# Performance work log

Hardware: AMD Instinct MI355X
Metric: run time of the kernel (lower is better)

The kernel has to match this reference:

```python
import jax, jax.numpy as jnp
import numpy as np

B, S, N, C = 8, 256, 256, 64
NH = 8
H, W = 256, 256
D = N * C // NH  # per-head channel dim = 2048
EPS = 1e-12


def window_reverse(windows, ws, Hh, Ww, Cc):
    # windows: (B, S, N, C) -> (B, H*W, C)
    b = windows.shape[0]
    x = windows.reshape(b, Hh // ws[0], Ww // ws[1], ws[0], ws[1], Cc)
    x = x.transpose(0, 1, 3, 2, 4, 5).reshape(b, Hh, Ww, Cc).reshape(b, Hh * Ww, Cc)
    return x


def window_partition(x, ws):
    # x: (B, H, W, C) -> (B, nWin, winElems, C)
    b, hh, ww, cc = x.shape
    x = x.reshape(b, hh // ws[0], ws[0], ww // ws[1], ws[1], cc)
    return x.transpose(0, 1, 3, 2, 4, 5).reshape(b, (hh // ws[0]) * (ww // ws[1]), ws[0] * ws[1], cc)


def setup_inputs() -> dict:
    key = jax.random.key(0)
    ks = jax.random.split(key, 6)
    x = jax.random.normal(ks[0], (B, S, N, C), dtype=jnp.float32)
    qkv_w = jax.random.normal(ks[1], (4 * C, C), dtype=jnp.float32) * 0.02
    qkv_b = jnp.zeros((4 * C,), dtype=jnp.float32)
    proj_w = jax.random.normal(ks[2], (C, C), dtype=jnp.float32) * 0.02
    proj_b = jnp.zeros((C,), dtype=jnp.float32)
    temperature1 = jnp.ones((NH, 1, 1), dtype=jnp.float32)
    temperature2 = jnp.ones((NH, 1, 1), dtype=jnp.float32)
    return {"x": x, "qkv_w": qkv_w, "qkv_b": qkv_b, "proj_w": proj_w,
            "proj_b": proj_b, "temperature1": temperature1, "temperature2": temperature2}


def reference(x, qkv_w, qkv_b, proj_w, proj_b, temperature1, temperature2):
    b, s, n, c = x.shape
    xf = x.reshape(b, s * n, c)
    # fused 4-way qkv projection (q, k, v_H, v_V)
    qkvv = (xf @ qkv_w.T + qkv_b).reshape(b, s, 4, NH, D).transpose(2, 0, 3, 1, 4)
    q, k, v_H, v_V = qkvv[0], qkvv[1], qkvv[2], qkvv[3]  # each (B, NH, S, D)

    # reorient v_V from H-windows (columns) to V-windows (rows)
    v_V = v_V.transpose(0, 2, 1, 3).reshape(b, s, n, c)       # (B,S,N,C)
    v_V = v_V.transpose(0, 2, 1, 3)                           # (B,N,S,C)
    v_V = window_reverse(v_V, (H, 1), H, W, c).reshape(b, H, W, c)
    v_V = window_partition(v_V, (1, W))                       # (B,H,W,C)
    v_V = v_V.transpose(0, 2, 1, 3)                           # (B,W,H,C) == (B,S,N,C)
    v_V = v_V.reshape(b, s, NH, D).transpose(0, 2, 1, 3)      # (B,NH,S,D)

    # cosine attention over S with per-head temperature
    qn = q / jnp.maximum(jnp.linalg.norm(q, axis=-1, keepdims=True), EPS)
    kn = k / jnp.maximum(jnp.linalg.norm(k, axis=-1, keepdims=True), EPS)
    sim = jnp.einsum('bhsd,bhtd->bhst', qn, kn)  # (B,NH,S,S)
    attn_H = jax.nn.softmax(sim * temperature1, axis=-1)
    attn_V = jax.nn.softmax(sim * temperature2, axis=-1)

    x_H = jnp.einsum('bhst,bhtd->bhsd', attn_H, v_H).transpose(0, 2, 1, 3).reshape(b, s * n, c)
    x_V = jnp.einsum('bhst,bhtd->bhsd', attn_V, v_V).transpose(0, 2, 1, 3).reshape(b, s * n, c)

    out = (x_H + x_V) @ proj_w.T + proj_b
    return out.reshape(b, s, n, c)
```

## Files before the change

kernel.cpp:

```cpp
#include <hip/hip_runtime.h>


using half_t = _Float16;
using half4 = __attribute__((ext_vector_type(4))) _Float16;
using half8 = __attribute__((ext_vector_type(8))) _Float16;
using f32x4 = __attribute__((ext_vector_type(4))) float;

#define NTOK 524288

#define GLDS(g, l) __builtin_amdgcn_global_load_lds( \
    (const __attribute__((address_space(1))) void*)(g), \
    (__attribute__((address_space(3))) void*)(l), 16, 0, 0)

#define WS_Q      0
#define WS_K      67108864
#define WS_VH     134217728
#define WS_VV     201326592
#define WS_XHV    268435456
#define WS_NQ     335544320
#define WS_NK     335609856
#define WS_WH     335675392
#define WS_WP     335708160

__global__ void kW0(const float* __restrict__ qkv_w, const float* __restrict__ proj_w,
                    half_t* __restrict__ Wh, half_t* __restrict__ Wp) {
    int tid = threadIdx.x;
    for (int i = tid; i < 256 * 64; i += 256) Wh[i] = (half_t)qkv_w[i];
    for (int i = tid; i < 64 * 64; i += 256) Wp[i] = (half_t)proj_w[i];
}

__device__ inline void y_tile_mfma(const float* __restrict__ xb,
                                   const half_t* __restrict__ Wh,
                                   int tbase, int hi, int lo,
                                   f32x4 (&acc)[4][4], int wave, int lane) {
    const int l15 = lane & 15, quad = lane >> 4;
#pragma unroll
    for (int kc = 0; kc < 2; ++kc) {
        const int c = kc * 32 + quad * 8;
        half8 afr[4];
#pragma unroll
        for (int mt = 0; mt < 4; ++mt) {
            int m = mt * 16 + l15;
            int token = tbase + (m >> 3) * hi + (m & 7) * lo;
            const float* p = xb + (size_t)token * 64 + c;
            f32x4 f0 = *(const f32x4*)p;
            f32x4 f1 = *(const f32x4*)(p + 4);
            half8 a;
            a[0] = (half_t)f0[0]; a[1] = (half_t)f0[1]; a[2] = (half_t)f0[2]; a[3] = (half_t)f0[3];
            a[4] = (half_t)f1[0]; a[5] = (half_t)f1[1]; a[6] = (half_t)f1[2]; a[7] = (half_t)f1[3];
            afr[mt] = a;
        }
#pragma unroll
        for (int i = 0; i < 4; ++i) {
            int j = (wave * 4 + i) * 16 + l15;
            half8 bfr = *(const half8*)(Wh + j * 64 + c);
#pragma unroll
            for (int mt = 0; mt < 4; ++mt)
                acc[mt][i] = __builtin_amdgcn_mfma_f32_16x16x32_f16(afr[mt], bfr, acc[mt][i], 0, 0, 0);
        }
    }
}

__device__ inline void y_tile_mfma_swapped(const float* __restrict__ xb,
                                           const half_t* __restrict__ Wh,
                                           int tbase, int hi, int lo,
                                           f32x4 (&acc)[4][4], int wave, int lane) {
    const int l15 = lane & 15, quad = lane >> 4;
#pragma unroll
    for (int kc = 0; kc < 2; ++kc) {
        const int c = kc * 32 + quad * 8;
        half8 bx[4];
#pragma unroll
        for (int mt = 0; mt < 4; ++mt) {
            int m = mt * 16 + l15;
            int token = tbase + (m >> 3) * hi + (m & 7) * lo;
            const float* p = xb + (size_t)token * 64 + c;
            f32x4 f0 = *(const f32x4*)p;
            f32x4 f1 = *(const f32x4*)(p + 4);
            half8 a;
            a[0] = (half_t)f0[0]; a[1] = (half_t)f0[1]; a[2] = (half_t)f0[2]; a[3] = (half_t)f0[3];
            a[4] = (half_t)f1[0]; a[5] = (half_t)f1[1]; a[6] = (half_t)f1[2]; a[7] = (half_t)f1[3];
            bx[mt] = a;
        }
#pragma unroll
        for (int i = 0; i < 4; ++i) {
            int j = (wave * 4 + i) * 16 + l15;
            half8 aw = *(const half8*)(Wh + j * 64 + c);
#pragma unroll
            for (int mt = 0; mt < 4; ++mt)
                acc[i][mt] = __builtin_amdgcn_mfma_f32_16x16x32_f16(aw, bx[mt], acc[i][mt], 0, 0, 0);
        }
    }
}

__device__ inline void y_dump_transposed(f32x4 (&acc)[4][4], const float* __restrict__ qkv_b,
                                         half_t* yldsT, int wave, int lane) {
    const int l15 = lane & 15, quad = lane >> 4;
#pragma unroll
    for (int i = 0; i < 4; ++i) {
        int j = (wave * 4 + i) * 16 + l15;
        float bj = qkv_b[j];
#pragma unroll
        for (int mt = 0; mt < 4; ++mt)
#pragma unroll
            for (int r = 0; r < 4; ++r)
                yldsT[j * 72 + mt * 16 + quad * 4 + r] = (half_t)(acc[mt][i][r] + bj);
    }
}

__global__ __launch_bounds__(256) void kA1(const float* __restrict__ x,
                                           const half_t* __restrict__ Wh,
                                           const float* __restrict__ qkv_b,
                                           half_t* __restrict__ Q, half_t* __restrict__ K,
                                           float* __restrict__ normQ, float* __restrict__ normK) {
    __shared__ half_t ylds[64 * 264];
    __shared__ float scr[256];
    int idx = blockIdx.x;
    int sb = idx & 31; idx >>= 5;
    int h = idx & 7; idx >>= 3;
    int g = idx & 1; int b = idx >> 1;
    int s0 = sb * 8;
    int n0 = g * 64 + h * 8;
    int tid = threadIdx.x, wave = tid >> 6, lane = tid & 63;
    const int l15 = lane & 15, quad = lane >> 4;
    const float* xb = x + (size_t)b * 65536 * 64;
    f32x4 acc[4][4];
#pragma unroll
    for (int a = 0; a < 4; ++a)
#pragma unroll
        for (int c = 0; c < 4; ++c) acc[a][c] = {0.f, 0.f, 0.f, 0.f};
    y_tile_mfma_swapped(xb, Wh, s0 * 256 + n0, 256, 1, acc, wave, lane);
#pragma unroll
    for (int i = 0; i < 4; ++i) {
        int j0 = (wave * 4 + i) * 16 + quad * 4;
        f32x4 bj = *(const f32x4*)&qkv_b[j0];
#pragma unroll
        for (int mt = 0; mt < 4; ++mt) {
            int m = mt * 16 + l15;
            half4 v;
#pragma unroll
            for (int r = 0; r < 4; ++r) v[r] = (half_t)(acc[i][mt][r] + bj[r]);
            *(half4*)&ylds[m * 264 + j0] = v;
        }
    }
    __syncthreads();
    half_t* dst = (g == 0 ? Q : K) + ((size_t)(b * 8 + h) * 256 + s0) * 2048;
    int ns = tid >> 5, jc = (tid & 31) * 8;
#pragma unroll
    for (int si = 0; si < 8; ++si) {
        half8 v = *(const half8*)&ylds[(si * 8 + ns) * 264 + jc];
        *(half8*)(dst + (size_t)si * 2048 + ns * 256 + jc) = v;
    }
    float sum = 0.f;
#pragma unroll
    for (int nn = 0; nn < 8; ++nn) {
        half8 v = *(const half8*)&ylds[((tid >> 5) * 8 + nn) * 264 + (tid & 31) * 8];
#pragma unroll
        for (int e = 0; e < 8; ++e) { float f = (float)v[e]; sum += f * f; }
    }
    scr[tid] = sum;
    __syncthreads();
    if (tid < 8) {
        float s = 0.f;
        for (int k2 = 0; k2 < 32; ++k2) s += scr[tid * 32 + k2];
        float* nd = (g == 0 ? normQ : normK);
        nd[(b * 8 + h) * 256 + s0 + tid] = s;
    }
}

__global__ __launch_bounds__(256) void kA2H(const float* __restrict__ x,
                                            const half_t* __restrict__ Wh,
                                            const float* __restrict__ qkv_b,
                                            half_t* __restrict__ VH) {
    __shared__ half_t yldsT[256 * 72];
    int idx = blockIdx.x;
    int sb = idx & 3; idx >>= 2;
    int nn = idx & 63; int b = idx >> 6;
    int h = nn >> 3, ns = nn & 7;
    int n = 128 + nn;
    int s0 = sb * 64;
    int tid = threadIdx.x, wave = tid >> 6, lane = tid & 63;
    const int l15 = lane & 15, quad = lane >> 4;
    const float* xb = x + (size_t)b * 65536 * 64;
    f32x4 acc[4][4];
#pragma unroll
    for (int a = 0; a < 4; ++a)
#pragma unroll
        for (int c = 0; c < 4; ++c) acc[a][c] = {0.f, 0.f, 0.f, 0.f};
    y_tile_mfma(xb, Wh, s0 * 256 + n, 2048, 256, acc, wave, lane);
#pragma unroll
    for (int i = 0; i < 4; ++i) {
        int j = (wave * 4 + i) * 16 + l15;
        float bj = qkv_b[j];
#pragma unroll
        for (int mt = 0; mt < 4; ++mt) {
            half4 v;
#pragma unroll
            for (int r = 0; r < 4; ++r) v[r] = (half_t)(acc[mt][i][r] + bj);
            *(half4*)&yldsT[j * 72 + mt * 16 + quad * 4] = v;
        }
    }
    __syncthreads();
    int jl = lane >> 3, tc = lane & 7;
    half_t* base = VH + ((size_t)(b * 8 + h) * 2048 + ns * 256) * 256 + s0 + tc * 8;
#pragma unroll
    for (int u = 0; u < 8; ++u) {
        int j = wave * 64 + u * 8 + jl;
        half8 v = *(const half8*)&yldsT[j * 72 + tc * 8];
        *(half8*)(base + (size_t)j * 256) = v;
    }
}

__global__ __launch_bounds__(256) void kA2V(const float* __restrict__ x,
                                            const half_t* __restrict__ Wh,
                                            const float* __restrict__ qkv_b,
                                            half_t* __restrict__ VV) {
    __shared__ half_t vlds[64 * 264];
    int idx = blockIdx.x;
    int st = idx & 255; int b = idx >> 8;
    int h = st >> 5;
    int tid = threadIdx.x, wave = tid >> 6, lane = tid & 63;
    const float* xb = x + (size_t)b * 65536 * 64;
    f32x4 acc[4][4];
#pragma unroll
    for (int a = 0; a < 4; ++a)
#pragma unroll
        for (int c = 0; c < 4; ++c) acc[a][c] = {0.f, 0.f, 0.f, 0.f};
    y_tile_mfma(xb, Wh, st * 256 + 192, 8, 1, acc, wave, lane);
    {
        const int l15 = lane & 15, quad = lane >> 4;
#pragma unroll
        for (int i = 0; i < 4; ++i) {
            int j = (wave * 4 + i) * 16 + l15;
            float bj = qkv_b[j];
            int dm = j & 63;
            int jc = j >> 6;
#pragma unroll
            for (int mt = 0; mt < 4; ++mt)
#pragma unroll
                for (int r = 0; r < 4; ++r) {
                    int m = mt * 16 + quad * 4 + r;
                    int t = 32 * (m >> 3) + 4 * (m & 7) + jc;
                    vlds[dm * 264 + t] = (half_t)(acc[mt][i][r] + bj);
                }
        }
    }
    __syncthreads();
    half_t* base = VV + ((size_t)(b * 8 + h) * 2048 + (st & 31) * 64) * 256;
    int l31 = lane & 31, lh = lane >> 5;
#pragma unroll
    for (int u = 0; u < 8; ++u) {
        int dm = u * 8 + wave * 2 + lh;
        half8 v = *(const half8*)&vlds[dm * 264 + l31 * 8];
        *(half8*)(base + (size_t)dm * 256 + l31 * 8) = v;
    }
}

__global__ __launch_bounds__(1024, 4) void kB(const half_t* __restrict__ Q, const half_t* __restrict__ K,
                                              const half_t* __restrict__ VH, const half_t* __restrict__ VV,
                                              const float* __restrict__ normQ, const float* __restrict__ normK,
                                              const float* __restrict__ temp1, const float* __restrict__ temp2,
                                              half_t* __restrict__ xhv) {
    extern __shared__ char smem[];
    half_t* PH = (half_t*)smem;
    half_t* PV = (half_t*)(smem + 40960);
    float* rq  = (float*)(smem + 122880);
    float* rk  = (float*)(smem + 123136);

    int idx = blockIdx.x;
    int bh = idx & 63;
    int sqb = idx >> 6;
    int h = bh & 7, b = bh >> 3;
    int sq0 = sqb * 64;
    int tid = threadIdx.x, wave = tid >> 6, lane = tid & 63;
    int l15 = lane & 15, quad = lane >> 4;
    float t1 = temp1[h], t2 = temp2[h];
    const half_t* Qb = Q + (size_t)bh * 256 * 2048;
    const half_t* Kb = K + (size_t)bh * 256 * 2048;
    const half_t* VHb = VH + (size_t)bh * 2048 * 256;
    const half_t* VVb = VV + (size_t)bh * 2048 * 256;

    if (tid < 64) rq[tid] = 1.f / fmaxf(sqrtf(normQ[bh * 256 + sq0 + tid]), 1e-12f);
    if (tid < 256) rk[tid] = 1.f / fmaxf(sqrtf(normK[bh * 256 + tid]), 1e-12f);

    {
        const int l7 = lane & 7, l8 = lane >> 3;
        const int swzh = (l7 ^ (l8 & 7)) * 8;
        const half_t* gK0 = Kb + (size_t)(wave * 8 + l8) * 2048 + swzh;
        const half_t* gK1 = Kb + (size_t)(128 + wave * 8 + l8) * 2048 + swzh;
        const half_t* gQ  = Qb + (size_t)(sq0 + (wave & 7) * 8 + l8) * 2048 + swzh;

        auto STAGE = [&](int kk, char* B) {
            const int off = kk * 64;
            GLDS(gK0 + off, B + wave * 1024);
            GLDS(gK1 + off, B + 16384 + wave * 1024);
            if (wave < 8) GLDS(gQ + off, B + 32768 + wave * 1024);
        };

        f32x4 acc1[4];
#pragma unroll
        for (int a = 0; a < 4; ++a) acc1[a] = {0.f, 0.f, 0.f, 0.f};
        const int tcol = wave * 16 + l15;
        const int ts7 = tcol & 7;

        auto COMPUTE = [&](const char* B) {
            const half_t* KsB = (const half_t*)B;
            const half_t* QsB = (const half_t*)(B + 32768);
#pragma unroll
            for (int sub = 0; sub < 2; ++sub) {
                int c16 = sub * 4 + quad;
                half8 bfr = *(const half8*)(KsB + tcol * 64 + (c16 ^ ts7) * 8);
#pragma unroll
                for (int mt = 0; mt < 4; ++mt) {
                    int m = mt * 16 + l15;
                    half8 afr = *(const half8*)(QsB + m * 64 + (c16 ^ (m & 7)) * 8);
                    acc1[mt] = __builtin_amdgcn_mfma_f32_16x16x32_f16(afr, bfr, acc1[mt], 0, 0, 0);
                }
            }
        };

        STAGE(0, smem);
        STAGE(1, smem + 40960);
        __syncthreads();
        int c0 = 0, c2 = 2;
        for (int kk = 0; kk < 30; ++kk) {
            COMPUTE(smem + c0 * 40960);
            STAGE(kk + 2, smem + c2 * 40960);
            if (wave < 8) { asm volatile("s_waitcnt vmcnt(3)" ::: "memory"); }
            else          { asm volatile("s_waitcnt vmcnt(2)" ::: "memory"); }
            __builtin_amdgcn_s_barrier();
            __builtin_amdgcn_sched_barrier(0);
            c0 = (c0 == 2) ? 0 : c0 + 1;
            c2 = (c2 == 2) ? 0 : c2 + 1;
        }
        COMPUTE(smem + c0 * 40960);
        asm volatile("s_waitcnt vmcnt(0)" ::: "memory");
        __builtin_amdgcn_s_barrier();
        __builtin_amdgcn_sched_barrier(0);
        c0 = (c0 == 2) ? 0 : c0 + 1;
        COMPUTE(smem + c0 * 40960);
        float rkt = rk[tcol];
#pragma unroll
        for (int mt = 0; mt < 4; ++mt)
#pragma unroll
            for (int r = 0; r < 4; ++r) {
                int row = mt * 16 + quad * 4 + r;
                PH[row * 264 + tcol] = (half_t)(acc1[mt][r] * rq[row] * rkt);
            }
    }
    __syncthreads();

    {
        int r_ = tid >> 4, cc = tid & 15;
        half_t* phrow = &PH[r_ * 264 + cc * 16];
        half_t* pvrow = &PV[r_ * 264 + cc * 16];
        half8 v0 = *(const half8*)phrow;
        half8 v1 = *(const half8*)(phrow + 8);
        float fv[16];
#pragma unroll
        for (int e = 0; e < 8; ++e) { fv[e] = (float)v0[e]; fv[8 + e] = (float)v1[e]; }
        float mx = fv[0], mn = fv[0];
#pragma unroll
        for (int e = 1; e < 16; ++e) { mx = fmaxf(mx, fv[e]); mn = fminf(mn, fv[e]); }
#pragma unroll
        for (int m = 1; m < 16; m <<= 1) {
            mx = fmaxf(mx, __shfl_xor(mx, m, 16));
            mn = fminf(mn, __shfl_xor(mn, m, 16));
        }
        float mh = (t1 >= 0.f) ? t1 * mx : t1 * mn;
        float mv = (t2 >= 0.f) ? t2 * mx : t2 * mn;
        float sh = 0.f, sv = 0.f;
#pragma unroll
        for (int e = 0; e < 16; ++e) {
            sh += __expf(fv[e] * t1 - mh);
            sv += __expf(fv[e] * t2 - mv);
        }
#pragma unroll
        for (int m = 1; m < 16; m <<= 1) {
            sh += __shfl_xor(sh, m, 16);
            sv += __shfl_xor(sv, m, 16);
        }
        float rh = 1.f / sh, rv = 1.f / sv;
        half8 o0, o1, p0, p1;
#pragma unroll
        for (int e = 0; e < 8; ++e) {
            o0[e] = (half_t)(__expf(fv[e] * t1 - mh) * rh);
            o1[e] = (half_t)(__expf(fv[8 + e] * t1 - mh) * rh);
            p0[e] = (half_t)(__expf(fv[e] * t2 - mv) * rv);
            p1[e] = (half_t)(__expf(fv[8 + e] * t2 - mv) * rv);
        }
        *(half8*)phrow = o0; *(half8*)(phrow + 8) = o1;
        *(half8*)pvrow = p0; *(half8*)(pvrow + 8) = p1;
    }
    __syncthreads();

    const int rr = lane >> 3, c8 = (lane & 7) * 8;
    half_t* myscr = (half_t*)(smem + 81920 + wave * 2560);
#pragma unroll
    for (int i2 = 0; i2 < 2; ++i2) {
        int d0 = wave * 64 + i2 * 1024;
        f32x4 acc2[4][4];
#pragma unroll
        for (int a = 0; a < 4; ++a)
#pragma unroll
            for (int c = 0; c < 4; ++c) acc2[a][c] = {0.f, 0.f, 0.f, 0.f};
        for (int kc = 0; kc < 8; ++kc) {
            int tk = kc * 32 + quad * 8;
            half8 afr[4];
#pragma unroll
            for (int mt = 0; mt < 4; ++mt)
                afr[mt] = *(const half8*)&PH[(mt * 16 + l15) * 264 + tk];
#pragma unroll
            for (int nt = 0; nt < 4; ++nt) {
                half8 bfr = *(const half8*)(VHb + (size_t)(d0 + nt * 16 + l15) * 256 + tk);
#pragma unroll
                for (int mt = 0; mt < 4; ++mt)
                    acc2[mt][nt] = __builtin_amdgcn_mfma_f32_16x16x32_f16(afr[mt], bfr, acc2[mt][nt], 0, 0, 0);
            }
#pragma unroll
            for (int mt = 0; mt < 4; ++mt)
                afr[mt] = *(const half8*)&PV[(mt * 16 + l15) * 264 + tk];
#pragma unroll
            for (int nt = 0; nt < 4; ++nt) {
                half8 bfr = *(const half8*)(VVb + (size_t)(d0 + nt * 16 + l15) * 256 + tk);
#pragma unroll
                for (int mt = 0; mt < 4; ++mt)
                    acc2[mt][nt] = __builtin_amdgcn_mfma_f32_16x16x32_f16(afr[mt], bfr, acc2[mt][nt], 0, 0, 0);
            }
        }
        int db = wave + i2 * 16;
        half_t* xbase = xhv + (((size_t)(b * 8 + h) * 32 + db) * 256 + sq0) * 64;
#pragma unroll
        for (int mt = 0; mt < 4; ++mt) {
#pragma unroll
            for (int nt = 0; nt < 4; ++nt)
#pragma unroll
                for (int r = 0; r < 4; ++r)
                    myscr[(quad * 4 + r) * 72 + nt * 16 + l15] = (half_t)acc2[mt][nt][r];
#pragma unroll
            for (int u = 0; u < 2; ++u) {
                half8 v = *(const half8*)&myscr[(u * 8 + rr) * 72 + c8];
                *(half8*)(xbase + (size_t)(mt * 16 + u * 8 + rr) * 64 + c8) = v;
            }
        }
    }
}

__global__ __launch_bounds__(256) void kC(const half_t* __restrict__ xhv, const half_t* __restrict__ Wp,
                                          const float* __restrict__ proj_b, float* __restrict__ out) {
    __shared__ float ot[64 * 68];
    int tid = threadIdx.x, wave = tid >> 6, lane = tid & 63;
    int l15 = lane & 15, quad = lane >> 4;
    size_t T0 = (size_t)blockIdx.x * 64;
    int b = (int)(T0 >> 16);
    int s = (int)((T0 >> 8) & 255);
    int n0 = (int)(T0 & 255);
    f32x4 acc[4];
#pragma unroll
    for (int a = 0; a < 4; ++a) acc[a] = {0.f, 0.f, 0.f, 0.f};
#pragma unroll
    for (int kc = 0; kc < 2; ++kc) {
        int c = kc * 32 + quad * 8;
        half8 bfr = *(const half8*)(Wp + (wave * 16 + l15) * 64 + c);
#pragma unroll
        for (int mt = 0; mt < 4; ++mt) {
            int n = n0 + mt * 16 + l15;
            int hh = n >> 5, db = n & 31;
            const half_t* arow = xhv + (((size_t)(b * 8 + hh) * 32 + db) * 256 + s) * 64;
            half8 afr = *(const half8*)(arow + c);
            acc[mt] = __builtin_amdgcn_mfma_f32_16x16x32_f16(afr, bfr, acc[mt], 0, 0, 0);
        }
    }
    float bj = proj_b[wave * 16 + l15];
#pragma unroll
    for (int mt = 0; mt < 4; ++mt)
#pragma unroll
        for (int r = 0; r < 4; ++r)
            ot[(mt * 16 + quad * 4 + r) * 68 + wave * 16 + l15] = acc[mt][r] + bj;
    __syncthreads();
    int row = tid >> 2;
#pragma unroll
    for (int u = 0; u < 4; ++u) {
        int col = (tid & 3) * 4 + u * 16;
        f32x4 v = *(const f32x4*)&ot[row * 68 + col];
        *(f32x4*)(out + (T0 + row) * 64 + col) = v;
    }
}

extern "C" void kernel_launch(void* const* d_in, const int* in_sizes, int n_in,
                              void* d_out, int out_size, void* d_ws, size_t ws_size,
                              hipStream_t stream) {
    const float* x      = (const float*)d_in[0];
    const float* qkv_w  = (const float*)d_in[1];
    const float* qkv_b  = (const float*)d_in[2];
    const float* proj_w = (const float*)d_in[3];
    const float* proj_b = (const float*)d_in[4];
    const float* temp1  = (const float*)d_in[5];
    const float* temp2  = (const float*)d_in[6];
    char* ws = (char*)d_ws;
    half_t* Q   = (half_t*)(ws + WS_Q);
    half_t* K   = (half_t*)(ws + WS_K);
    half_t* VH  = (half_t*)(ws + WS_VH);
    half_t* VV  = (half_t*)(ws + WS_VV);
    half_t* xhv = (half_t*)(ws + WS_XHV);
    float* normQ = (float*)(ws + WS_NQ);
    float* normK = (float*)(ws + WS_NK);
    half_t* Wh  = (half_t*)(ws + WS_WH);
    half_t* Wp  = (half_t*)(ws + WS_WP);
    float* out = (float*)d_out;

    hipFuncSetAttribute((const void*)kB, hipFuncAttributeMaxDynamicSharedMemorySize, 124160);

    kW0<<<1, 256, 0, stream>>>(qkv_w, proj_w, Wh, Wp);
    kA1<<<4096, 256, 0, stream>>>(x, Wh, qkv_b, Q, K, normQ, normK);
    kA2H<<<2048, 256, 0, stream>>>(x, Wh, qkv_b, VH);
    kA2V<<<2048, 256, 0, stream>>>(x, Wh, qkv_b, VV);
    kB<<<256, 1024, 124160, stream>>>(Q, K, VH, VV, normQ, normK, temp1, temp2, xhv);
    kC<<<8192, 256, 0, stream>>>(xhv, Wp, proj_b, out);
}
```

Before: 586.3 us.

## Pre-convert x to fp16 and merge projection kernels into one launch

Adds a pass that converts all of x to fp16 into the workspace (reusing the xhv region) while also converting the weights. The three projection kernels are merged into one 8192-block kernel that reads fp16 x, halving gather traffic and dropping the conversion work inside each block. Norm accumulation is now done in registers with wave shuffles instead of an LDS re-read. The cost is an extra full pass that reads x in fp32 and writes it as fp16, and the per-token norm is now taken from fp32 values instead of fp16-rounded ones.

```diff
diff --git a/kernel.cpp b/kernel.cpp
--- a/kernel.cpp
+++ b/kernel.cpp
@@ -22,213 +22,198 @@
 #define WS_WH     335675392
 #define WS_WP     335708160
 
-__global__ void kW0(const float* __restrict__ qkv_w, const float* __restrict__ proj_w,
-                    half_t* __restrict__ Wh, half_t* __restrict__ Wp) {
+__global__ __launch_bounds__(256) void kX(const float* __restrict__ x, half_t* __restrict__ xh,
+                                          const float* __restrict__ qkv_w, const float* __restrict__ proj_w,
+                                          half_t* __restrict__ Wh, half_t* __restrict__ Wp) {
     int tid = threadIdx.x;
-    for (int i = tid; i < 256 * 64; i += 256) Wh[i] = (half_t)qkv_w[i];
-    for (int i = tid; i < 64 * 64; i += 256) Wp[i] = (half_t)proj_w[i];
+    if (blockIdx.x == 0) {
+        for (int i = tid; i < 256 * 64; i += 256) Wh[i] = (half_t)qkv_w[i];
+        for (int i = tid; i < 64 * 64; i += 256) Wp[i] = (half_t)proj_w[i];
+    }
+    for (size_t i = (size_t)blockIdx.x * 256 + tid; i < 4194304u; i += 524288u) {
+        const float* p = x + i * 8;
+        f32x4 f0 = *(const f32x4*)p;
+        f32x4 f1 = *(const f32x4*)(p + 4);
+        half8 v;
+        v[0] = (half_t)f0[0]; v[1] = (half_t)f0[1]; v[2] = (half_t)f0[2]; v[3] = (half_t)f0[3];
+        v[4] = (half_t)f1[0]; v[5] = (half_t)f1[1]; v[6] = (half_t)f1[2]; v[7] = (half_t)f1[3];
+        *(half8*)(xh + i * 8) = v;
+    }
 }
 
-__device__ inline void y_tile_mfma(const float* __restrict__ xb,
-                                   const half_t* __restrict__ Wh,
-                                   int tbase, int hi, int lo,
-                                   f32x4 (&acc)[4][4], int wave, int lane) {
+__global__ __launch_bounds__(256) void kA(const half_t* __restrict__ xh,
+                                          const half_t* __restrict__ Wh,
+                                          const float* __restrict__ qkv_b,
+                                          half_t* __restrict__ Q, half_t* __restrict__ K,
+                                          half_t* __restrict__ VH, half_t* __restrict__ VV,
+                                          float* __restrict__ normQ, float* __restrict__ normK) {
+    __shared__ __align__(16) char smem[36992];
+    int tid = threadIdx.x, wave = tid >> 6, lane = tid & 63;
     const int l15 = lane & 15, quad = lane >> 4;
-#pragma unroll
-    for (int kc = 0; kc < 2; ++kc) {
-        const int c = kc * 32 + quad * 8;
-        half8 afr[4];
+    int idx = blockIdx.x;
+
+    if (idx < 4096) {
+        half_t* ylds = (half_t*)smem;
+        float* scr = (float*)(smem + 33792);
+        int sb = idx & 31; idx >>= 5;
+        int h = idx & 7; idx >>= 3;
+        int g = idx & 1; int b = idx >> 1;
+        int s0 = sb * 8;
+        int n0 = g * 64 + h * 8;
+        const half_t* xb = xh + (size_t)b * 65536 * 64;
+        const int tbase = s0 * 256 + n0;
+        f32x4 acc[4][4];
+#pragma unroll
+        for (int a = 0; a < 4; ++a)
+#pragma unroll
+            for (int c = 0; c < 4; ++c) acc[a][c] = {0.f, 0.f, 0.f, 0.f};
+#pragma unroll
+        for (int kc = 0; kc < 2; ++kc) {
+            const int c = kc * 32 + quad * 8;
+            half8 bx[4];
+#pragma unroll
+            for (int mt = 0; mt < 4; ++mt) {
+                int m = mt * 16 + l15;
+                int token = tbase + (m >> 3) * 256 + (m & 7);
+                bx[mt] = *(const half8*)(xb + (size_t)token * 64 + c);
+            }
+#pragma unroll
+            for (int i = 0; i < 4; ++i) {
+                int j = (wave * 4 + i) * 16 + l15;
+                half8 aw = *(const half8*)(Wh + j * 64 + c);
+#pragma unroll
+                for (int mt = 0; mt < 4; ++mt)
+                    acc[i][mt] = __builtin_amdgcn_mfma_f32_16x16x32_f16(aw, bx[mt], acc[i][mt], 0, 0, 0);
+            }
+        }
+        float nsum[4] = {0.f, 0.f, 0.f, 0.f};
+#pragma unroll
+        for (int i = 0; i < 4; ++i) {
+            int j0 = (wave * 4 + i) * 16 + quad * 4;
+            f32x4 bj = *(const f32x4*)&qkv_b[j0];
+#pragma unroll
+            for (int mt = 0; mt < 4; ++mt) {
+                half4 v;
+#pragma unroll
+                for (int r = 0; r < 4; ++r) {
+                    float f = acc[i][mt][r] + bj[r];
+                    v[r] = (half_t)f;
+                    nsum[mt] += f * f;
+                }
+                *(half4*)&ylds[(mt * 16 + l15) * 264 + j0] = v;
+            }
+        }
 #pragma unroll
         for (int mt = 0; mt < 4; ++mt) {
-            int m = mt * 16 + l15;
-            int token = tbase + (m >> 3) * hi + (m & 7) * lo;
-            const float* p = xb + (size_t)token * 64 + c;
-            f32x4 f0 = *(const f32x4*)p;
-            f32x4 f1 = *(const f32x4*)(p + 4);
-            half8 a;
-            a[0] = (half_t)f0[0]; a[1] = (half_t)f0[1]; a[2] = (half_t)f0[2]; a[3] = (half_t)f0[3];
-            a[4] = (half_t)f1[0]; a[5] = (half_t)f1[1]; a[6] = (half_t)f1[2]; a[7] = (half_t)f1[3];
-            afr[mt] = a;
+            float v = nsum[mt];
+            v += __shfl_xor(v, 1);  v += __shfl_xor(v, 2);  v += __shfl_xor(v, 4);
+            v += __shfl_xor(v, 16); v += __shfl_xor(v, 32);
+            nsum[mt] = v;
+        }
+        if (lane == 0 || lane == 8) {
+#pragma unroll
+            for (int mt = 0; mt < 4; ++mt)
+                scr[wave * 8 + mt * 2 + (lane >> 3)] = nsum[mt];
+        }
+        __syncthreads();
+        half_t* dst = (g == 0 ? Q : K) + ((size_t)(b * 8 + h) * 256 + s0) * 2048;
+        int ns = tid >> 5, jc = (tid & 31) * 8;
+#pragma unroll
+        for (int si = 0; si < 8; ++si) {
+            half8 v = *(const half8*)&ylds[(si * 8 + ns) * 264 + jc];
+            *(half8*)(dst + (size_t)si * 2048 + ns * 256 + jc) = v;
+        }
+        if (tid < 8) {
+            float s = scr[tid] + scr[8 + tid] + scr[16 + tid] + scr[24 + tid];
+            float* nd = (g == 0 ? normQ : normK);
+            nd[(b * 8 + h) * 256 + s0 + tid] = s;
+        }
+    } else if (idx < 6144) {
+        half_t* yldsT = (half_t*)smem;
+        int id2 = idx - 4096;
+        int sb = id2 & 3; id2 >>= 2;
+        int nn = id2 & 63; int b = id2 >> 6;
+        int h = nn >> 3, ns = nn & 7;
+        int n = 128 + nn;
+        int s0 = sb * 64;
+        const half_t* xb = xh + (size_t)b * 65536 * 64;
+        const int tbase = s0 * 256 + n;
+        f32x4 acc[4][4];
+#pragma unroll
+        for (int a = 0; a < 4; ++a)
+#pragma unroll
+            for (int c = 0; c < 4; ++c) acc[a][c] = {0.f, 0.f, 0.f, 0.f};
+#pragma unroll
+        for (int kc = 0; kc < 2; ++kc) {
+            const int c = kc * 32 + quad * 8;
+            half8 afr[4];
+#pragma unroll
+            for (int mt = 0; mt < 4; ++mt) {
+                int m = mt * 16 + l15;
+                int token = tbase + (m >> 3) * 2048 + (m & 7) * 256;
+                afr[mt] = *(const half8*)(xb + (size_t)token * 64 + c);
+            }
+#pragma unroll
+            for (int i = 0; i < 4; ++i) {
+                int j = (wave * 4 + i) * 16 + l15;
+                half8 bfr = *(const half8*)(Wh + j * 64 + c);
+#pragma unroll
+                for (int mt = 0; mt < 4; ++mt)
+                    acc[mt][i] = __builtin_amdgcn_mfma_f32_16x16x32_f16(afr[mt], bfr, acc[mt][i], 0, 0, 0);
+            }
         }
 #pragma unroll
         for (int i = 0; i < 4; ++i) {
             int j = (wave * 4 + i) * 16 + l15;
-            half8 bfr = *(const half8*)(Wh + j * 64 + c);
-#pragma unroll
-            for (int mt = 0; mt < 4; ++mt)
-                acc[mt][i] = __builtin_amdgcn_mfma_f32_16x16x32_f16(afr[mt], bfr, acc[mt][i], 0, 0, 0);
-        }
-    }
-}
-
-__device__ inline void y_tile_mfma_swapped(const float* __restrict__ xb,
-                                           const half_t* __restrict__ Wh,
-                                           int tbase, int hi, int lo,
-                                           f32x4 (&acc)[4][4], int wave, int lane) {
-    const int l15 = lane & 15, quad = lane >> 4;
-#pragma unroll
-    for (int kc = 0; kc < 2; ++kc) {
-        const int c = kc * 32 + quad * 8;
-        half8 bx[4];
-#pragma unroll
-        for (int mt = 0; mt < 4; ++mt) {
-            int m = mt * 16 + l15;
-            int token = tbase + (m >> 3) * hi + (m & 7) * lo;
-            const float* p = xb + (size_t)token * 64 + c;
-            f32x4 f0 = *(const f32x4*)p;
-            f32x4 f1 = *(const f32x4*)(p + 4);
-            half8 a;
-            a[0] = (half_t)f0[0]; a[1] = (half_t)f0[1]; a[2] = (half_t)f0[2]; a[3] = (half_t)f0[3];
-            a[4] = (half_t)f1[0]; a[5] = (half_t)f1[1]; a[6] = (half_t)f1[2]; a[7] = (half_t)f1[3];
-            bx[mt] = a;
-        }
-#pragma unroll
-        for (int i = 0; i < 4; ++i) {
-            int j = (wave * 4 + i) * 16 + l15;
-            half8 aw = *(const half8*)(Wh + j * 64 + c);
-#pragma unroll
-            for (int mt = 0; mt < 4; ++mt)
-                acc[i][mt] = __builtin_amdgcn_mfma_f32_16x16x32_f16(aw, bx[mt], acc[i][mt], 0, 0, 0);
-        }
-    }
-}
-
-__device__ inline void y_dump_transposed(f32x4 (&acc)[4][4], const float* __restrict__ qkv_b,
-                                         half_t* yldsT, int wave, int lane) {
-    const int l15 = lane & 15, quad = lane >> 4;
-#pragma unroll
-    for (int i = 0; i < 4; ++i) {
-        int j = (wave * 4 + i) * 16 + l15;
-        float bj = qkv_b[j];
-#pragma unroll
-        for (int mt = 0; mt < 4; ++mt)
-#pragma unroll
-            for (int r = 0; r < 4; ++r)
-                yldsT[j * 72 + mt * 16 + quad * 4 + r] = (half_t)(acc[mt][i][r] + bj);
-    }
-}
-
-__global__ __launch_bounds__(256) void kA1(const float* __restrict__ x,
-                                           const half_t* __restrict__ Wh,
-                                           const float* __restrict__ qkv_b,
-                                           half_t* __restrict__ Q, half_t* __restrict__ K,
-                                           float* __restrict__ normQ, float* __restrict__ normK) {
-    __shared__ half_t ylds[64 * 264];
-    __shared__ float scr[256];
-    int idx = blockIdx.x;
-    int sb = idx & 31; idx >>= 5;
-    int h = idx & 7; idx >>= 3;
-    int g = idx & 1; int b = idx >> 1;
-    int s0 = sb * 8;
-    int n0 = g * 64 + h * 8;
-    int tid = threadIdx.x, wave = tid >> 6, lane = tid & 63;
-    const int l15 = lane & 15, quad = lane >> 4;
-    const float* xb = x + (size_t)b * 65536 * 64;
-    f32x4 acc[4][4];
-#pragma unroll
-    for (int a = 0; a < 4; ++a)
-#pragma unroll
-        for (int c = 0; c < 4; ++c) acc[a][c] = {0.f, 0.f, 0.f, 0.f};
-    y_tile_mfma_swapped(xb, Wh, s0 * 256 + n0, 256, 1, acc, wave, lane);
-#pragma unroll
-    for (int i = 0; i < 4; ++i) {
-        int j0 = (wave * 4 + i) * 16 + quad * 4;
-        f32x4 bj = *(const f32x4*)&qkv_b[j0];
-#pragma unroll
-        for (int mt = 0; mt < 4; ++mt) {
-            int m = mt * 16 + l15;
-            half4 v;
-#pragma unroll
-            for (int r = 0; r < 4; ++r) v[r] = (half_t)(acc[i][mt][r] + bj[r]);
-            *(half4*)&ylds[m * 264 + j0] = v;
-        }
-    }
-    __syncthreads();
-    half_t* dst = (g == 0 ? Q : K) + ((size_t)(b * 8 + h) * 256 + s0) * 2048;
-    int ns = tid >> 5, jc = (tid & 31) * 8;
-#pragma unroll
-    for (int si = 0; si < 8; ++si) {
-        half8 v = *(const half8*)&ylds[(si * 8 + ns) * 264 + jc];
-        *(half8*)(dst + (size_t)si * 2048 + ns * 256 + jc) = v;
-    }
-    float sum = 0.f;
-#pragma unroll
-    for (int nn = 0; nn < 8; ++nn) {
-        half8 v = *(const half8*)&ylds[((tid >> 5) * 8 + nn) * 264 + (tid & 31) * 8];
-#pragma unroll
-        for (int e = 0; e < 8; ++e) { float f = (float)v[e]; sum += f * f; }
-    }
-    scr[tid] = sum;
-    __syncthreads();
-    if (tid < 8) {
-        float s = 0.f;
-        for (int k2 = 0; k2 < 32; ++k2) s += scr[tid * 32 + k2];
-        float* nd = (g == 0 ? normQ : normK);
-        nd[(b * 8 + h) * 256 + s0 + tid] = s;
-    }
-}
-
-__global__ __launch_bounds__(256) void kA2H(const float* __restrict__ x,
-                                            const half_t* __restrict__ Wh,
-                                            const float* __restrict__ qkv_b,
-                                            half_t* __restrict__ VH) {
-    __shared__ half_t yldsT[256 * 72];
-    int idx = blockIdx.x;
-    int sb = idx & 3; idx >>= 2;
-    int nn = idx & 63; int b = idx >> 6;
-    int h = nn >> 3, ns = nn & 7;
-    int n = 128 + nn;
-    int s0 = sb * 64;
-    int tid = threadIdx.x, wave = tid >> 6, lane = tid & 63;
-    const int l15 = lane & 15, quad = lane >> 4;
-    const float* xb = x + (size_t)b * 65536 * 64;
-    f32x4 acc[4][4];
-#pragma unroll
-    for (int a = 0; a < 4; ++a)
-#pragma unroll
-        for (int c = 0; c < 4; ++c) acc[a][c] = {0.f, 0.f, 0.f, 0.f};
-    y_tile_mfma(xb, Wh, s0 * 256 + n, 2048, 256, acc, wave, lane);
-#pragma unroll
-    for (int i = 0; i < 4; ++i) {
-        int j = (wave * 4 + i) * 16 + l15;
-        float bj = qkv_b[j];
-#pragma unroll
-        for (int mt = 0; mt < 4; ++mt) {
-            half4 v;
-#pragma unroll
-            for (int r = 0; r < 4; ++r) v[r] = (half_t)(acc[mt][i][r] + bj);
-            *(half4*)&yldsT[j * 72 + mt * 16 + quad * 4] = v;
-        }
-    }
-    __syncthreads();
-    int jl = lane >> 3, tc = lane & 7;
-    half_t* base = VH + ((size_t)(b * 8 + h) * 2048 + ns * 256) * 256 + s0 + tc * 8;
-#pragma unroll
-    for (int u = 0; u < 8; ++u) {
-        int j = wave * 64 + u * 8 + jl;
-        half8 v = *(const half8*)&yldsT[j * 72 + tc * 8];
-        *(half8*)(base + (size_t)j * 256) = v;
-    }
-}
-
-__global__ __launch_bounds__(256) void kA2V(const float* __restrict__ x,
-                                            const half_t* __restrict__ Wh,
-                                            const float* __restrict__ qkv_b,
-                                            half_t* __restrict__ VV) {
-    __shared__ half_t vlds[64 * 264];
-    int idx = blockIdx.x;
-    int st = idx & 255; int b = idx >> 8;
-    int h = st >> 5;
-    int tid = threadIdx.x, wave = tid >> 6, lane = tid & 63;
-    const float* xb = x + (size_t)b * 65536 * 64;
-    f32x4 acc[4][4];
-#pragma unroll
-    for (int a = 0; a < 4; ++a)
-#pragma unroll
-        for (int c = 0; c < 4; ++c) acc[a][c] = {0.f, 0.f, 0.f, 0.f};
-    y_tile_mfma(xb, Wh, st * 256 + 192, 8, 1, acc, wave, lane);
-    {
-        const int l15 = lane & 15, quad = lane >> 4;
+            float bj = qkv_b[j];
+#pragma unroll
+            for (int mt = 0; mt < 4; ++mt) {
+                half4 v;
+#pragma unroll
+                for (int r = 0; r < 4; ++r) v[r] = (half_t)(acc[mt][i][r] + bj);
+                *(half4*)&yldsT[j * 72 + mt * 16 + quad * 4] = v;
+            }
+        }
+        __syncthreads();
+        int jl = lane >> 3, tc = lane & 7;
+        half_t* base = VH + ((size_t)(b * 8 + h) * 2048 + ns * 256) * 256 + s0 + tc * 8;
+#pragma unroll
+        for (int u = 0; u < 8; ++u) {
+            int j = wave * 64 + u * 8 + jl;
+            half8 v = *(const half8*)&yldsT[j * 72 + tc * 8];
+            *(half8*)(base + (size_t)j * 256) = v;
+        }
+    } else {
+        half_t* vlds = (half_t*)smem;
+        int id2 = idx - 6144;
+        int st = id2 & 255; int b = id2 >> 8;
+        int h = st >> 5;
+        const half_t* xb = xh + (size_t)b * 65536 * 64;
+        const int tbase = st * 256 + 192;
+        f32x4 acc[4][4];
+#pragma unroll
+        for (int a = 0; a < 4; ++a)
+#pragma unroll
+            for (int c = 0; c < 4; ++c) acc[a][c] = {0.f, 0.f, 0.f, 0.f};
+#pragma unroll
+        for (int kc = 0; kc < 2; ++kc) {
+            const int c = kc * 32 + quad * 8;
+            half8 afr[4];
+#pragma unroll
+            for (int mt = 0; mt < 4; ++mt) {
+                int m = mt * 16 + l15;
+                int token = tbase + (m >> 3) * 8 + (m & 7);
+                afr[mt] = *(const half8*)(xb + (size_t)token * 64 + c);
+            }
+#pragma unroll
+            for (int i = 0; i < 4; ++i) {
+                int j = (wave * 4 + i) * 16 + l15;
+                half8 bfr = *(const half8*)(Wh + j * 64 + c);
+#pragma unroll
+                for (int mt = 0; mt < 4; ++mt)
+                    acc[mt][i] = __builtin_amdgcn_mfma_f32_16x16x32_f16(afr[mt], bfr, acc[mt][i], 0, 0, 0);
+            }
+        }
 #pragma unroll
         for (int i = 0; i < 4; ++i) {
             int j = (wave * 4 + i) * 16 + l15;
@@ -244,15 +229,15 @@
                     vlds[dm * 264 + t] = (half_t)(acc[mt][i][r] + bj);
                 }
         }
-    }
-    __syncthreads();
-    half_t* base = VV + ((size_t)(b * 8 + h) * 2048 + (st & 31) * 64) * 256;
-    int l31 = lane & 31, lh = lane >> 5;
-#pragma unroll
-    for (int u = 0; u < 8; ++u) {
-        int dm = u * 8 + wave * 2 + lh;
-        half8 v = *(const half8*)&vlds[dm * 264 + l31 * 8];
-        *(half8*)(base + (size_t)dm * 256 + l31 * 8) = v;
+        __syncthreads();
+        half_t* base = VV + ((size_t)(b * 8 + h) * 2048 + (st & 31) * 64) * 256;
+        int l31 = lane & 31, lh = lane >> 5;
+#pragma unroll
+        for (int u = 0; u < 8; ++u) {
+            int dm = u * 8 + wave * 2 + lh;
+            half8 v = *(const half8*)&vlds[dm * 264 + l31 * 8];
+            *(half8*)(base + (size_t)dm * 256 + l31 * 8) = v;
+        }
     }
 }
 
@@ -502,6 +487,7 @@
     half_t* K   = (half_t*)(ws + WS_K);
     half_t* VH  = (half_t*)(ws + WS_VH);
     half_t* VV  = (half_t*)(ws + WS_VV);
+    half_t* xh  = (half_t*)(ws + WS_XHV);
     half_t* xhv = (half_t*)(ws + WS_XHV);
     float* normQ = (float*)(ws + WS_NQ);
     float* normK = (float*)(ws + WS_NK);
@@ -511,10 +497,8 @@
 
     hipFuncSetAttribute((const void*)kB, hipFuncAttributeMaxDynamicSharedMemorySize, 124160);
 
-    kW0<<<1, 256, 0, stream>>>(qkv_w, proj_w, Wh, Wp);
-    kA1<<<4096, 256, 0, stream>>>(x, Wh, qkv_b, Q, K, normQ, normK);
-    kA2H<<<2048, 256, 0, stream>>>(x, Wh, qkv_b, VH);
-    kA2V<<<2048, 256, 0, stream>>>(x, Wh, qkv_b, VV);
+    kX<<<2048, 256, 0, stream>>>(x, xh, qkv_w, proj_w, Wh, Wp);
+    kA<<<8192, 256, 0, stream>>>(xh, Wh, qkv_b, Q, K, VH, VV, normQ, normK);
     kB<<<256, 1024, 124160, stream>>>(Q, K, VH, VV, normQ, normK, temp1, temp2, xhv);
     kC<<<8192, 256, 0, stream>>>(xhv, Wp, proj_b, out);
 }
```

New measurement: 563.6 us. 1.04x faster.
